# Optimization experiments

Measured on AMD Instinct MI355X. Metric: run time of the kernel, lower is better.

## Reference

```python
import jax, jax.numpy as jnp
import numpy as np
import math

PI = math.pi

def setup_inputs() -> dict:
    key = jax.random.key(0)
    ks = jax.random.split(key, 12)
    B, L, D, K = 2, 2048, 256, 32
    s = 0.02
    return {
        "x":   jax.random.normal(ks[0], (B, L, D), dtype=jnp.float32),
        "kw1": jax.random.normal(ks[1], (D, D), dtype=jnp.float32) * s,
        "kb1": jnp.zeros((D,), dtype=jnp.float32),
        "kw2": jax.random.normal(ks[2], (K, D), dtype=jnp.float32) * s,
        "kb2": jnp.zeros((K,), dtype=jnp.float32),
        "qw1": jax.random.normal(ks[3], (D, D), dtype=jnp.float32) * s,
        "qb1": jnp.zeros((D,), dtype=jnp.float32),
        "qw2": jax.random.normal(ks[4], (K, D), dtype=jnp.float32) * s,
        "qb2": jnp.zeros((K,), dtype=jnp.float32),
        "vw":  jax.random.normal(ks[5], (D, D), dtype=jnp.float32) * s,
        "vb":  jnp.zeros((D,), dtype=jnp.float32),
    }

def _encode_phase(x, w1, b1, w2, b2):
    # Sequential(Linear, Tanh, Linear) followed by outer tanh * pi in forward
    h = jnp.tanh(jnp.einsum('bld,ed->ble', x, w1) + b1)
    return jnp.tanh(jnp.einsum('bld,kd->blk', h, w2) + b2) * PI

def reference(x, kw1, kb1, kw2, kb2, qw1, qb1, qw2, qb2, vw, vb):
    B, L, D = x.shape
    key_phase = _encode_phase(x, kw1, kb1, kw2, kb2)    # [B,L,K]
    query_phase = _encode_phase(x, qw1, qb1, qw2, qb2)  # [B,L,K]
    K = key_phase.shape[-1]
    value = jnp.einsum('bld,ed->ble', x, vw) + vb       # [B,L,D]

    cos_k = jnp.cos(key_phase)[..., None]               # [B,L,K,1]
    sin_k = jnp.sin(key_phase)[..., None]
    v_exp = value[:, :, None, :]                        # [B,L,1,D]
    mem_real = jnp.cumsum(cos_k * v_exp, axis=1)        # [B,L,K,D]
    mem_imag = jnp.cumsum(sin_k * v_exp, axis=1)

    cos_q = jnp.cos(query_phase)[..., None]
    sin_q = jnp.sin(query_phase)[..., None]
    retrieved = jnp.sum(mem_real * cos_q + mem_imag * sin_q, axis=2)  # [B,L,D]

    positions = jnp.arange(1, L + 1, dtype=x.dtype)
    norm = jnp.sqrt(positions * K)[None, :, None]
    return retrieved / norm
```

## Files before the change

### kernel.cpp

```cpp
#include <hip/hip_runtime.h>
#include <hip/hip_bf16.h>
#include <math.h>

typedef float v4f   __attribute__((ext_vector_type(4)));
typedef float f32x4 __attribute__((ext_vector_type(4)));
typedef short s16x8 __attribute__((ext_vector_type(8)));
typedef __hip_bfloat16 bf16;

#define PI_F 3.14159265358979323846f


__device__ inline unsigned short f2bf(float f) {
    unsigned int b = __float_as_uint(f);
    unsigned int r = (b + 0x7FFFu + ((b >> 16) & 1u)) >> 16;
    return (unsigned short)r;
}
__device__ inline float bf2f(unsigned short u) {
    return __uint_as_float(((unsigned int)u) << 16);
}
__device__ inline void cvt8(const float* __restrict__ src, unsigned short* dst) {
    v4f a = *(const v4f*)src, b = *(const v4f*)(src + 4);
    ushort4 u0, u1;
    u0.x = f2bf(a[0]); u0.y = f2bf(a[1]); u0.z = f2bf(a[2]); u0.w = f2bf(a[3]);
    u1.x = f2bf(b[0]); u1.y = f2bf(b[1]); u1.z = f2bf(b[2]); u1.w = f2bf(b[3]);
    *(ushort4*)dst = u0; *(ushort4*)(dst + 4) = u1;
}

__global__ __launch_bounds__(256) void k_cvtw(
    const float* __restrict__ kw1, const float* __restrict__ qw1,
    const float* __restrict__ vw,  const float* __restrict__ kw2,
    const float* __restrict__ qw2, bf16* __restrict__ Wb, bf16* __restrict__ W2b)
{
    int i8 = blockIdx.x * 256 + threadIdx.x;
    int r = i8 >> 5, c8 = (i8 & 31) * 8;
    const float* src;
    unsigned short* dst;
    if (r < 768) {
        src = (r < 256) ? kw1 + (size_t)r * 256
            : (r < 512) ? qw1 + (size_t)(r - 256) * 256
                        : vw  + (size_t)(r - 512) * 256;
        dst = (unsigned short*)Wb + (size_t)r * 256;
    } else {
        int r2 = r - 768;
        src = (r2 < 32) ? kw2 + (size_t)r2 * 256 : qw2 + (size_t)(r2 - 32) * 256;
        dst = (unsigned short*)W2b + (size_t)r2 * 256;
    }
    cvt8(src + c8, dst + c8);
}

__global__ __launch_bounds__(1024) void k_fused1(
    const float* __restrict__ X,   const bf16* __restrict__ Wbk,
    const float* __restrict__ kb1, const float* __restrict__ qb1,
    const float* __restrict__ vb,  const bf16* __restrict__ W2bk,
    const float* __restrict__ kb2, const float* __restrict__ qb2,
    float* __restrict__ KP, float* __restrict__ QP,
    bf16* __restrict__ Vb, bf16* __restrict__ SRg, bf16* __restrict__ SIg)
{
    __shared__ __align__(16) unsigned char smem[58880];
    unsigned short* Abf = (unsigned short*)smem;
    unsigned short* Vt  = (unsigned short*)smem;
    unsigned short* CKc = (unsigned short*)(smem + 20480);
    unsigned short* CKs = (unsigned short*)(smem + 23040);
    unsigned short* Hkq = (unsigned short*)(smem + 25600);

    const int tid  = threadIdx.x;
    const int lane = tid & 63, wid = tid >> 6;
    const int lrow = lane & 15, lk8 = (lane >> 4) * 8;
    const int t0   = (lane >> 4) * 4;
    const int bb = blockIdx.x >> 6, cc = blockIdx.x & 63;
    const int row0 = bb * 2048 + cc * 32;

    {
        int r = tid >> 5, c8 = (tid & 31) * 8;
        cvt8(X + (size_t)(row0 + r) * 256 + c8, &Abf[r * 264 + c8]);
    }
    __syncthreads();

    const int nb = wid * 48;
    const unsigned short* Wu = (const unsigned short*)Wbk;
    f32x4 acc[2][3] = {};
    for (int k0 = 0; k0 < 256; k0 += 32) {
        s16x8 a[2], b[3];
        #pragma unroll
        for (int mf = 0; mf < 2; ++mf)
            a[mf] = *(const s16x8*)&Abf[(mf * 16 + lrow) * 264 + k0 + lk8];
        #pragma unroll
        for (int nf = 0; nf < 3; ++nf)
            b[nf] = *(const s16x8*)(Wu + (size_t)(nb + nf * 16 + lrow) * 256 + k0 + lk8);
        #pragma unroll
        for (int mf = 0; mf < 2; ++mf)
            #pragma unroll
            for (int nf = 0; nf < 3; ++nf)
                acc[mf][nf] = __builtin_amdgcn_mfma_f32_16x16x32_bf16(
                    a[mf], b[nf], acc[mf][nf], 0, 0, 0);
    }
    __syncthreads();

    #pragma unroll
    for (int nf = 0; nf < 3; ++nf) {
        int n = nb + nf * 16 + lrow;
        float bias = (n < 256) ? kb1[n] : (n < 512) ? qb1[n - 256] : vb[n - 512];
        #pragma unroll
        for (int mf = 0; mf < 2; ++mf) {
            int tb = mf * 16 + t0;
            if (n < 512) {
                #pragma unroll
                for (int r = 0; r < 4; ++r)
                    Hkq[(tb + r) * 520 + n] = f2bf(tanhf(acc[mf][nf][r] + bias));
            } else {
                int d = n - 512;
                float v0 = acc[mf][nf][0] + bias, v1 = acc[mf][nf][1] + bias;
                float v2 = acc[mf][nf][2] + bias, v3 = acc[mf][nf][3] + bias;
                ushort4 u;
                u.x = f2bf(v0); u.y = f2bf(v1); u.z = f2bf(v2); u.w = f2bf(v3);
                *(ushort4*)&Vt[d * 40 + tb] = u;
                unsigned short* Vg = (unsigned short*)Vb + (size_t)(row0 + tb) * 256 + d;
                Vg[0] = u.x; Vg[256] = u.y; Vg[512] = u.z; Vg[768] = u.w;
            }
        }
    }
    __syncthreads();

    if (wid < 8) {
        const int which = wid >> 2;
        const int q = wid & 3, mf = q >> 1, nf = q & 1;
        const int hoff = which * 256;
        const unsigned short* W2u =
            (const unsigned short*)W2bk + (size_t)(which * 32 + nf * 16 + lrow) * 256;
        f32x4 u = {};
        for (int k0 = 0; k0 < 256; k0 += 32) {
            s16x8 a = *(const s16x8*)&Hkq[(mf * 16 + lrow) * 520 + hoff + k0 + lk8];
            s16x8 b = *(const s16x8*)(W2u + k0 + lk8);
            u = __builtin_amdgcn_mfma_f32_16x16x32_bf16(a, b, u, 0, 0, 0);
        }
        const int outk = nf * 16 + lrow;
        const float bias = (which ? qb2 : kb2)[outk];
        float* dst = which ? QP : KP;
        float cs[4], sn[4];
        #pragma unroll
        for (int r = 0; r < 4; ++r) {
            float ph = tanhf(u[r] + bias) * PI_F;
            float s, c_;
            __sincosf(ph, &s, &c_);
            cs[r] = c_; sn[r] = s;
            int row = mf * 16 + t0 + r;
            dst[(size_t)(row0 + row) * 64 + outk]      = c_;
            dst[(size_t)(row0 + row) * 64 + 32 + outk] = s;
        }
        if (which == 0) {
            ushort4 uc, us;
            uc.x = f2bf(cs[0]); uc.y = f2bf(cs[1]); uc.z = f2bf(cs[2]); uc.w = f2bf(cs[3]);
            us.x = f2bf(sn[0]); us.y = f2bf(sn[1]); us.z = f2bf(sn[2]); us.w = f2bf(sn[3]);
            *(ushort4*)&CKc[outk * 40 + mf * 16 + t0] = uc;
            *(ushort4*)&CKs[outk * 40 + mf * 16 + t0] = us;
        }
    }
    __syncthreads();

    {
        s16x8 bV = *(const s16x8*)&Vt[(wid * 16 + lrow) * 40 + lk8];
        s16x8 c0 = *(const s16x8*)&CKc[(lrow) * 40 + lk8];
        s16x8 c1 = *(const s16x8*)&CKc[(16 + lrow) * 40 + lk8];
        s16x8 s0 = *(const s16x8*)&CKs[(lrow) * 40 + lk8];
        s16x8 s1 = *(const s16x8*)&CKs[(16 + lrow) * 40 + lk8];
        f32x4 z = {};
        f32x4 r0 = __builtin_amdgcn_mfma_f32_16x16x32_bf16(c0, bV, z, 0, 0, 0);
        f32x4 r1 = __builtin_amdgcn_mfma_f32_16x16x32_bf16(c1, bV, z, 0, 0, 0);
        f32x4 i0 = __builtin_amdgcn_mfma_f32_16x16x32_bf16(s0, bV, z, 0, 0, 0);
        f32x4 i1 = __builtin_amdgcn_mfma_f32_16x16x32_bf16(s1, bV, z, 0, 0, 0);
        const int d = wid * 16 + lrow;
        size_t base = (((size_t)(bb * 64 + cc)) * 32) * 256 + d;
        unsigned short* SRu = (unsigned short*)SRg;
        unsigned short* SIu = (unsigned short*)SIg;
        #pragma unroll
        for (int r = 0; r < 4; ++r) {
            int ka = t0 + r, kb_ = 16 + t0 + r;
            SRu[base + (size_t)ka  * 256] = f2bf(r0[r]);
            SRu[base + (size_t)kb_ * 256] = f2bf(r1[r]);
            SIu[base + (size_t)ka  * 256] = f2bf(i0[r]);
            SIu[base + (size_t)kb_ * 256] = f2bf(i1[r]);
        }
    }
}

__global__ __launch_bounds__(256) void k_scanpart(
    const bf16* __restrict__ SRg, const bf16* __restrict__ SIg,
    float* __restrict__ PSR, float* __restrict__ PSI)
{
    const unsigned short* S = (const unsigned short*)(blockIdx.y ? SIg : SRg);
    float* PS = blockIdx.y ? PSI : PSR;
    int gid = blockIdx.x * 256 + threadIdx.x;
    int b = gid >> 14, seg = (gid >> 12) & 3, e2 = gid & 4095;
    size_t base = ((size_t)(b * 64 + seg * 16)) * 8192 + e2 * 2;
    float s0 = 0.f, s1 = 0.f;
    #pragma unroll
    for (int c = 0; c < 16; ++c) {
        ushort2 u = *(const ushort2*)(S + base + (size_t)c * 8192);
        s0 += bf2f(u.x); s1 += bf2f(u.y);
    }
    size_t pb = ((size_t)(b * 4 + seg)) * 8192 + e2 * 2;
    PS[pb] = s0; PS[pb + 1] = s1;
}

__global__ __launch_bounds__(256) void k_attnout(
    const float* __restrict__ KP, const float* __restrict__ QP,
    const bf16* __restrict__ Vb,
    const bf16* __restrict__ SRg, const bf16* __restrict__ SIg,
    const float* __restrict__ PSR, const float* __restrict__ PSI,
    float* __restrict__ out)
{
    __shared__ float QPc[32 * 68], KPc[32 * 68], Sl[32 * 36];
    __shared__ float vall[32 * 68], PRl[32 * 68], PIl[32 * 68];
    const int tid = threadIdx.x;
    const int b = blockIdx.x >> 6, c = blockIdx.x & 63;
    const int dh = blockIdx.y;
    const int row0 = b * 2048 + c * 32;

    #pragma unroll
    for (int it = 0; it < 2; ++it) {
        int idx = tid + it * 256, t = idx >> 4, j4 = idx & 15;
        *(v4f*)&QPc[t * 68 + j4 * 4] = *(const v4f*)(QP + (size_t)(row0 + t) * 64 + j4 * 4);
        *(v4f*)&KPc[t * 68 + j4 * 4] = *(const v4f*)(KP + (size_t)(row0 + t) * 64 + j4 * 4);
    }
    {
        int t = tid >> 3, e8 = (tid & 7) * 8;
        s16x8 u = *(const s16x8*)((const unsigned short*)Vb
                                  + (size_t)(row0 + t) * 256 + dh * 64 + e8);
        #pragma unroll
        for (int j = 0; j < 8; ++j) vall[t * 68 + e8 + j] = bf2f((unsigned short)u[j]);
    }
    {
        int k = tid >> 3, dg = tid & 7;
        float pr[8] = {}, pi[8] = {};
        int seg = c >> 4;
        for (int s = 0; s < seg; ++s) {
            size_t pb = ((size_t)(b * 4 + s)) * 8192 + k * 256 + dh * 64 + dg * 8;
            v4f r0 = *(const v4f*)(PSR + pb), r1 = *(const v4f*)(PSR + pb + 4);
            v4f i0 = *(const v4f*)(PSI + pb), i1 = *(const v4f*)(PSI + pb + 4);
            #pragma unroll
            for (int j = 0; j < 4; ++j) {
                pr[j] += r0[j]; pr[4 + j] += r1[j];
                pi[j] += i0[j]; pi[4 + j] += i1[j];
            }
        }
        for (int cp = (seg << 4); cp < c; ++cp) {
            size_t sb = (((size_t)(b * 64 + cp)) * 32 + k) * 256 + dh * 64 + dg * 8;
            s16x8 ur = *(const s16x8*)((const unsigned short*)SRg + sb);
            s16x8 ui = *(const s16x8*)((const unsigned short*)SIg + sb);
            #pragma unroll
            for (int j = 0; j < 8; ++j) {
                pr[j] += bf2f((unsigned short)ur[j]);
                pi[j] += bf2f((unsigned short)ui[j]);
            }
        }
        #pragma unroll
        for (int j = 0; j < 8; ++j) {
            PRl[k * 68 + dg * 8 + j] = pr[j];
            PIl[k * 68 + dg * 8 + j] = pi[j];
        }
    }
    __syncthreads();
    {
        const int sl = tid >> 3, tq = tid & 7;
        float s4[4] = {0.f, 0.f, 0.f, 0.f};
        for (int j4 = 0; j4 < 16; ++j4) {
            v4f q4 = *(const v4f*)&QPc[sl * 68 + j4 * 4];
            #pragma unroll
            for (int i = 0; i < 4; ++i) {
                v4f k4 = *(const v4f*)&KPc[(tq * 4 + i) * 68 + j4 * 4];
                s4[i] += q4[0]*k4[0] + q4[1]*k4[1] + q4[2]*k4[2] + q4[3]*k4[3];
            }
        }
        #pragma unroll
        for (int i = 0; i < 4; ++i) {
            int t = tq * 4 + i;
            Sl[sl * 36 + t] = (t <= sl) ? s4[i] : 0.f;
        }
    }
    __syncthreads();
    const int l = tid & 31, dq = tid >> 5;
    const int d0 = dq * 8;
    float acc[8] = {};
    for (int k = 0; k < 32; ++k) {
        float qc = QPc[l * 68 + k], qs = QPc[l * 68 + 32 + k];
        #pragma unroll
        for (int j4 = 0; j4 < 2; ++j4) {
            v4f pr = *(const v4f*)&PRl[k * 68 + d0 + j4 * 4];
            v4f pi = *(const v4f*)&PIl[k * 68 + d0 + j4 * 4];
            #pragma unroll
            for (int x = 0; x < 4; ++x)
                acc[j4 * 4 + x] += qc * pr[x] + qs * pi[x];
        }
    }
    for (int t = 0; t < 32; ++t) {
        float s = Sl[l * 36 + t];
        #pragma unroll
        for (int j4 = 0; j4 < 2; ++j4) {
            v4f v4 = *(const v4f*)&vall[t * 68 + d0 + j4 * 4];
            #pragma unroll
            for (int x = 0; x < 4; ++x)
                acc[j4 * 4 + x] = fmaf(s, v4[x], acc[j4 * 4 + x]);
        }
    }
    const int gl = c * 32 + l;
    const float inv = rsqrtf((float)((gl + 1) * 32));
    const size_t ob = ((size_t)(b * 2048 + gl)) * 256 + dh * 64 + d0;
    #pragma unroll
    for (int j4 = 0; j4 < 2; ++j4) {
        v4f v;
        #pragma unroll
        for (int x = 0; x < 4; ++x) v[x] = acc[j4 * 4 + x] * inv;
        *(v4f*)(out + ob + j4 * 4) = v;
    }
}

extern "C" void kernel_launch(void* const* d_in, const int* in_sizes, int n_in,
                              void* d_out, int out_size, void* d_ws, size_t ws_size,
                              hipStream_t stream)
{
    const float* x   = (const float*)d_in[0];
    const float* kw1 = (const float*)d_in[1];
    const float* kb1 = (const float*)d_in[2];
    const float* kw2 = (const float*)d_in[3];
    const float* kb2 = (const float*)d_in[4];
    const float* qw1 = (const float*)d_in[5];
    const float* qb1 = (const float*)d_in[6];
    const float* qw2 = (const float*)d_in[7];
    const float* qb2 = (const float*)d_in[8];
    const float* vw  = (const float*)d_in[9];
    const float* vb  = (const float*)d_in[10];
    float* out = (float*)d_out;

    char* ws = (char*)d_ws;
    float* KP  = (float*)ws;   ws += (size_t)4096 * 64 * 4;
    float* QP  = (float*)ws;   ws += (size_t)4096 * 64 * 4;
    float* PSR = (float*)ws;   ws += (size_t)65536 * 4;
    float* PSI = (float*)ws;   ws += (size_t)65536 * 4;
    bf16*  Wb  = (bf16*)ws;    ws += (size_t)768 * 256 * 2;
    bf16*  W2b = (bf16*)ws;    ws += (size_t)64 * 256 * 2;
    bf16*  Vb  = (bf16*)ws;    ws += (size_t)4096 * 256 * 2;
    bf16*  SR  = (bf16*)ws;    ws += (size_t)2 * 64 * 32 * 256 * 2;
    bf16*  SI  = (bf16*)ws;    ws += (size_t)2 * 64 * 32 * 256 * 2;

    k_cvtw    <<<104,          256,  0, stream>>>(kw1, qw1, vw, kw2, qw2, Wb, W2b);
    k_fused1  <<<128,          1024, 0, stream>>>(x, Wb, kb1, qb1, vb, W2b, kb2, qb2,
                                                  KP, QP, Vb, SR, SI);
    k_scanpart<<<dim3(128, 2), 256,  0, stream>>>(SR, SI, PSR, PSI);
    k_attnout <<<dim3(128, 4), 256,  0, stream>>>(KP, QP, Vb, SR, SI, PSR, PSI, out);
}
```

Before: 51.80 us.

## Fold weight conversion into encode kernel and drop separate segment-scan kernel

Removes the standalone weight fp32-to-bf16 conversion kernel; the encode kernel now loads fp32 weights directly and packs them to bf16 in registers before each MFMA. Also removes the partial-sum scan kernel; the output kernel now sums all preceding chunk summaries itself, up to 63 chunks, instead of combining segment partials. This cuts the launch count from four to two. In exchange each of the 128 encode blocks re-reads fp32 weights at twice the bytes and converts them redundantly, and later chunks in the output kernel do more serial loads.

```diff
diff --git a/kernel.cpp b/kernel.cpp
--- a/kernel.cpp
+++ b/kernel.cpp
@@ -25,34 +25,23 @@
     u1.x = f2bf(b[0]); u1.y = f2bf(b[1]); u1.z = f2bf(b[2]); u1.w = f2bf(b[3]);
     *(ushort4*)dst = u0; *(ushort4*)(dst + 4) = u1;
 }
-
-__global__ __launch_bounds__(256) void k_cvtw(
-    const float* __restrict__ kw1, const float* __restrict__ qw1,
-    const float* __restrict__ vw,  const float* __restrict__ kw2,
-    const float* __restrict__ qw2, bf16* __restrict__ Wb, bf16* __restrict__ W2b)
-{
-    int i8 = blockIdx.x * 256 + threadIdx.x;
-    int r = i8 >> 5, c8 = (i8 & 31) * 8;
-    const float* src;
-    unsigned short* dst;
-    if (r < 768) {
-        src = (r < 256) ? kw1 + (size_t)r * 256
-            : (r < 512) ? qw1 + (size_t)(r - 256) * 256
-                        : vw  + (size_t)(r - 512) * 256;
-        dst = (unsigned short*)Wb + (size_t)r * 256;
-    } else {
-        int r2 = r - 768;
-        src = (r2 < 32) ? kw2 + (size_t)r2 * 256 : qw2 + (size_t)(r2 - 32) * 256;
-        dst = (unsigned short*)W2b + (size_t)r2 * 256;
-    }
-    cvt8(src + c8, dst + c8);
-}
-
-__global__ __launch_bounds__(1024) void k_fused1(
-    const float* __restrict__ X,   const bf16* __restrict__ Wbk,
-    const float* __restrict__ kb1, const float* __restrict__ qb1,
-    const float* __restrict__ vb,  const bf16* __restrict__ W2bk,
-    const float* __restrict__ kb2, const float* __restrict__ qb2,
+__device__ inline s16x8 pack_bf8(const float* __restrict__ p) {
+    v4f w0 = *(const v4f*)p, w1 = *(const v4f*)(p + 4);
+    s16x8 b;
+    b[0] = (short)f2bf(w0[0]); b[1] = (short)f2bf(w0[1]);
+    b[2] = (short)f2bf(w0[2]); b[3] = (short)f2bf(w0[3]);
+    b[4] = (short)f2bf(w1[0]); b[5] = (short)f2bf(w1[1]);
+    b[6] = (short)f2bf(w1[2]); b[7] = (short)f2bf(w1[3]);
+    return b;
+}
+
+__global__ __launch_bounds__(1024) void k_encode(
+    const float* __restrict__ X,
+    const float* __restrict__ kw1, const float* __restrict__ kb1,
+    const float* __restrict__ kw2, const float* __restrict__ kb2,
+    const float* __restrict__ qw1, const float* __restrict__ qb1,
+    const float* __restrict__ qw2, const float* __restrict__ qb2,
+    const float* __restrict__ vw,  const float* __restrict__ vb,
     float* __restrict__ KP, float* __restrict__ QP,
     bf16* __restrict__ Vb, bf16* __restrict__ SRg, bf16* __restrict__ SIg)
 {
@@ -77,7 +66,16 @@
     __syncthreads();
 
     const int nb = wid * 48;
-    const unsigned short* Wu = (const unsigned short*)Wbk;
+    const float* wrow[3];
+    float bias1[3];
+    #pragma unroll
+    for (int nf = 0; nf < 3; ++nf) {
+        int n = nb + nf * 16 + lrow;
+        wrow[nf]  = (n < 256) ? kw1 + (size_t)n * 256
+                  : (n < 512) ? qw1 + (size_t)(n - 256) * 256
+                              : vw  + (size_t)(n - 512) * 256;
+        bias1[nf] = (n < 256) ? kb1[n] : (n < 512) ? qb1[n - 256] : vb[n - 512];
+    }
     f32x4 acc[2][3] = {};
     for (int k0 = 0; k0 < 256; k0 += 32) {
         s16x8 a[2], b[3];
@@ -86,7 +84,7 @@
             a[mf] = *(const s16x8*)&Abf[(mf * 16 + lrow) * 264 + k0 + lk8];
         #pragma unroll
         for (int nf = 0; nf < 3; ++nf)
-            b[nf] = *(const s16x8*)(Wu + (size_t)(nb + nf * 16 + lrow) * 256 + k0 + lk8);
+            b[nf] = pack_bf8(wrow[nf] + k0 + lk8);
         #pragma unroll
         for (int mf = 0; mf < 2; ++mf)
             #pragma unroll
@@ -99,7 +97,7 @@
     #pragma unroll
     for (int nf = 0; nf < 3; ++nf) {
         int n = nb + nf * 16 + lrow;
-        float bias = (n < 256) ? kb1[n] : (n < 512) ? qb1[n - 256] : vb[n - 512];
+        float bias = bias1[nf];
         #pragma unroll
         for (int mf = 0; mf < 2; ++mf) {
             int tb = mf * 16 + t0;
@@ -125,13 +123,12 @@
         const int which = wid >> 2;
         const int q = wid & 3, mf = q >> 1, nf = q & 1;
         const int hoff = which * 256;
-        const unsigned short* W2u =
-            (const unsigned short*)W2bk + (size_t)(which * 32 + nf * 16 + lrow) * 256;
+        const float* W2row = (which ? qw2 : kw2) + (size_t)(nf * 16 + lrow) * 256;
         f32x4 u = {};
         for (int k0 = 0; k0 < 256; k0 += 32) {
             s16x8 a = *(const s16x8*)&Hkq[(mf * 16 + lrow) * 520 + hoff + k0 + lk8];
-            s16x8 b = *(const s16x8*)(W2u + k0 + lk8);
-            u = __builtin_amdgcn_mfma_f32_16x16x32_bf16(a, b, u, 0, 0, 0);
+            u = __builtin_amdgcn_mfma_f32_16x16x32_bf16(
+                a, pack_bf8(W2row + k0 + lk8), u, 0, 0, 0);
         }
         const int outk = nf * 16 + lrow;
         const float bias = (which ? qb2 : kb2)[outk];
@@ -183,30 +180,10 @@
     }
 }
 
-__global__ __launch_bounds__(256) void k_scanpart(
-    const bf16* __restrict__ SRg, const bf16* __restrict__ SIg,
-    float* __restrict__ PSR, float* __restrict__ PSI)
-{
-    const unsigned short* S = (const unsigned short*)(blockIdx.y ? SIg : SRg);
-    float* PS = blockIdx.y ? PSI : PSR;
-    int gid = blockIdx.x * 256 + threadIdx.x;
-    int b = gid >> 14, seg = (gid >> 12) & 3, e2 = gid & 4095;
-    size_t base = ((size_t)(b * 64 + seg * 16)) * 8192 + e2 * 2;
-    float s0 = 0.f, s1 = 0.f;
-    #pragma unroll
-    for (int c = 0; c < 16; ++c) {
-        ushort2 u = *(const ushort2*)(S + base + (size_t)c * 8192);
-        s0 += bf2f(u.x); s1 += bf2f(u.y);
-    }
-    size_t pb = ((size_t)(b * 4 + seg)) * 8192 + e2 * 2;
-    PS[pb] = s0; PS[pb + 1] = s1;
-}
-
 __global__ __launch_bounds__(256) void k_attnout(
     const float* __restrict__ KP, const float* __restrict__ QP,
     const bf16* __restrict__ Vb,
     const bf16* __restrict__ SRg, const bf16* __restrict__ SIg,
-    const float* __restrict__ PSR, const float* __restrict__ PSI,
     float* __restrict__ out)
 {
     __shared__ float QPc[32 * 68], KPc[32 * 68], Sl[32 * 36];
@@ -232,21 +209,13 @@
     {
         int k = tid >> 3, dg = tid & 7;
         float pr[8] = {}, pi[8] = {};
-        int seg = c >> 4;
-        for (int s = 0; s < seg; ++s) {
-            size_t pb = ((size_t)(b * 4 + s)) * 8192 + k * 256 + dh * 64 + dg * 8;
-            v4f r0 = *(const v4f*)(PSR + pb), r1 = *(const v4f*)(PSR + pb + 4);
-            v4f i0 = *(const v4f*)(PSI + pb), i1 = *(const v4f*)(PSI + pb + 4);
-            #pragma unroll
-            for (int j = 0; j < 4; ++j) {
-                pr[j] += r0[j]; pr[4 + j] += r1[j];
-                pi[j] += i0[j]; pi[4 + j] += i1[j];
-            }
-        }
-        for (int cp = (seg << 4); cp < c; ++cp) {
-            size_t sb = (((size_t)(b * 64 + cp)) * 32 + k) * 256 + dh * 64 + dg * 8;
-            s16x8 ur = *(const s16x8*)((const unsigned short*)SRg + sb);
-            s16x8 ui = *(const s16x8*)((const unsigned short*)SIg + sb);
+        const unsigned short* SRu = (const unsigned short*)SRg;
+        const unsigned short* SIu = (const unsigned short*)SIg;
+        size_t sb = ((size_t)(b * 64) * 32 + k) * 256 + dh * 64 + dg * 8;
+        #pragma unroll 4
+        for (int cp = 0; cp < c; ++cp) {
+            s16x8 ur = *(const s16x8*)(SRu + sb + (size_t)cp * 8192);
+            s16x8 ui = *(const s16x8*)(SIu + sb + (size_t)cp * 8192);
             #pragma unroll
             for (int j = 0; j < 8; ++j) {
                 pr[j] += bf2f((unsigned short)ur[j]);
@@ -296,10 +265,10 @@
         float s = Sl[l * 36 + t];
         #pragma unroll
         for (int j4 = 0; j4 < 2; ++j4) {
-            v4f v4 = *(const v4f*)&vall[t * 68 + d0 + j4 * 4];
+            v4f v4_ = *(const v4f*)&vall[t * 68 + d0 + j4 * 4];
             #pragma unroll
             for (int x = 0; x < 4; ++x)
-                acc[j4 * 4 + x] = fmaf(s, v4[x], acc[j4 * 4 + x]);
+                acc[j4 * 4 + x] = fmaf(s, v4_[x], acc[j4 * 4 + x]);
         }
     }
     const int gl = c * 32 + l;
@@ -332,19 +301,14 @@
     float* out = (float*)d_out;
 
     char* ws = (char*)d_ws;
-    float* KP  = (float*)ws;   ws += (size_t)4096 * 64 * 4;
-    float* QP  = (float*)ws;   ws += (size_t)4096 * 64 * 4;
-    float* PSR = (float*)ws;   ws += (size_t)65536 * 4;
-    float* PSI = (float*)ws;   ws += (size_t)65536 * 4;
-    bf16*  Wb  = (bf16*)ws;    ws += (size_t)768 * 256 * 2;
-    bf16*  W2b = (bf16*)ws;    ws += (size_t)64 * 256 * 2;
-    bf16*  Vb  = (bf16*)ws;    ws += (size_t)4096 * 256 * 2;
-    bf16*  SR  = (bf16*)ws;    ws += (size_t)2 * 64 * 32 * 256 * 2;
-    bf16*  SI  = (bf16*)ws;    ws += (size_t)2 * 64 * 32 * 256 * 2;
-
-    k_cvtw    <<<104,          256,  0, stream>>>(kw1, qw1, vw, kw2, qw2, Wb, W2b);
-    k_fused1  <<<128,          1024, 0, stream>>>(x, Wb, kb1, qb1, vb, W2b, kb2, qb2,
-                                                  KP, QP, Vb, SR, SI);
-    k_scanpart<<<dim3(128, 2), 256,  0, stream>>>(SR, SI, PSR, PSI);
-    k_attnout <<<dim3(128, 4), 256,  0, stream>>>(KP, QP, Vb, SR, SI, PSR, PSI, out);
-}
+    float* KP = (float*)ws; ws += (size_t)4096 * 64 * 4;
+    float* QP = (float*)ws; ws += (size_t)4096 * 64 * 4;
+    bf16*  Vb = (bf16*)ws;  ws += (size_t)4096 * 256 * 2;
+    bf16*  SR = (bf16*)ws;  ws += (size_t)2 * 64 * 32 * 256 * 2;
+    bf16*  SI = (bf16*)ws;  ws += (size_t)2 * 64 * 32 * 256 * 2;
+
+    k_encode <<<128,          1024, 0, stream>>>(x, kw1, kb1, kw2, kb2,
+                                                 qw1, qb1, qw2, qb2, vw, vb,
+                                                 KP, QP, Vb, SR, SI);
+    k_attnout<<<dim3(128, 4), 256,  0, stream>>>(KP, QP, Vb, SR, SI, out);
+}
```

Result: slower. 59.83 us (+15.5%).
